# Optimization experiments

Measured on AMD Instinct MI355X. Metric: run time of the kernel, lower is better.

Reference implementation:

```python
import jax, jax.numpy as jnp
import numpy as np
from jax import lax

# NOTE: ResidualConvBlock and SS2DChanelFirst are reconstructed from the repo's
# conventions: ResidualConvBlock = act(conv3x3 -> act -> conv3x3 + 1x1 skip);
# SS2DChanelFirst = standard VMamba SS2D (in_proj -> dw-conv3x3 -> SiLU ->
# 4-direction cross-scan selective scan -> cross-merge -> LayerNorm -> *SiLU(z)
# gate -> out_proj) operating on NCHW tensors.

B, CIN, H, W = 4, 6, 64, 64
DM, DI, K, N, R, NL, GROUPS = 72, 144, 4, 8, 4, 2, 12


def conv2d(x, w, b=None, groups=1):
    out = lax.conv_general_dilated(x, w, (1, 1), 'SAME',
                                   dimension_numbers=('NCHW', 'OIHW', 'NCHW'),
                                   feature_group_count=groups)
    if b is not None:
        out = out + b[None, :, None, None]
    return out


def lrelu(x, s):
    return jnp.where(x >= 0, x, s * x)


def selective_scan(u, delta, A, Bs, Cs, D):
    # u, delta: (b,K,C,L); A: (K,C,N); Bs, Cs: (b,K,N,L); D: (K,C)
    b, k, c, l = u.shape
    n = A.shape[-1]
    ul = jnp.moveaxis(u, -1, 0)
    dl = jnp.moveaxis(delta, -1, 0)
    Bl = jnp.moveaxis(Bs, -1, 0)
    Cl = jnp.moveaxis(Cs, -1, 0)
    h0 = jnp.zeros((b, k, c, n), u.dtype)

    def step(h, xt):
        d_t, u_t, B_t, C_t = xt
        h = h * jnp.exp(d_t[..., None] * A) + (d_t * u_t)[..., None] * B_t[:, :, None, :]
        return h, jnp.einsum('bkcn,bkn->bkc', h, C_t)

    _, ys = lax.scan(step, h0, (dl, ul, Bl, Cl))
    return jnp.moveaxis(ys, 0, -1) + u * D[None, :, :, None]


def ss2d(x, in_w, dw_w, dw_b, xp_w, dtp_w, dtp_b, A_logs, Ds, ong, onb, op_w):
    b, dm, h_, w_ = x.shape
    l = h_ * w_
    xz = jnp.einsum('ec,bchw->behw', in_w, x)  # (b, 2*DI, h, w)
    xi, z = xz[:, :DI], xz[:, DI:]
    xi = jax.nn.silu(conv2d(xi, dw_w, dw_b, groups=DI))
    # cross-scan: row-major, col-major, and their reverses
    x0 = xi.reshape(b, DI, l)
    x1 = jnp.swapaxes(xi, 2, 3).reshape(b, DI, l)
    xs = jnp.stack([x0, x1, x0[..., ::-1], x1[..., ::-1]], axis=1)  # (b,4,DI,l)
    x_dbl = jnp.einsum('bkdl,kcd->bkcl', xs, xp_w)  # (b,4,R+2N,l)
    dts, Bs, Cs = x_dbl[:, :, :R], x_dbl[:, :, R:R + N], x_dbl[:, :, R + N:]
    dts = jnp.einsum('bkrl,kdr->bkdl', dts, dtp_w)
    delta = jax.nn.softplus(dts + dtp_b[None, :, :, None])
    A = -jnp.exp(A_logs).reshape(K, DI, N)
    ys = selective_scan(xs, delta, A, Bs, Cs, Ds.reshape(K, DI))  # (b,4,DI,l)
    # cross-merge
    y = ys[:, 0] + ys[:, 2, :, ::-1]
    yt = ys[:, 1] + ys[:, 3, :, ::-1]
    y = y + jnp.swapaxes(yt.reshape(b, DI, w_, h_), 2, 3).reshape(b, DI, l)
    y = jnp.swapaxes(y, 1, 2)  # (b,l,DI)
    mu = y.mean(-1, keepdims=True)
    var = ((y - mu) ** 2).mean(-1, keepdims=True)
    y = (y - mu) / jnp.sqrt(var + 1e-5) * ong + onb
    y = y * jax.nn.silu(jnp.swapaxes(z.reshape(b, DI, l), 1, 2))
    out = jnp.einsum('bld,ed->ble', y, op_w)  # (b,l,DM)
    return jnp.swapaxes(out, 1, 2).reshape(b, dm, h_, w_)


def groupnorm(x, g, bta, groups):
    b, c, h_, w_ = x.shape
    xg = x.reshape(b, groups, c // groups, h_ * w_)
    mu = xg.mean((2, 3), keepdims=True)
    var = ((xg - mu) ** 2).mean((2, 3), keepdims=True)
    xg = (xg - mu) / jnp.sqrt(var + 1e-5)
    return xg.reshape(b, c, h_, w_) * g[None, :, None, None] + bta[None, :, None, None]


def setup_inputs() -> dict:
    key = jax.random.key(0)
    ks = iter(jax.random.split(key, 32))
    nrm = lambda shp, s=0.05: jax.random.normal(next(ks), shp, jnp.float32) * s
    inp = {
        'image': jax.random.normal(next(ks), (B, CIN, H, W), jnp.float32),
        'cb_w1': nrm((DM, CIN, 3, 3), 0.1), 'cb_b1': nrm((DM,), 0.02),
        'cb_w2': nrm((DM, DM, 3, 3), 0.05), 'cb_b2': nrm((DM,), 0.02),
        'cb_ws': nrm((DM, CIN, 1, 1), 0.1), 'cb_bs': nrm((DM,), 0.02),
        'in_w': nrm((NL, 2 * DI, DM), 0.05),
        'dw_w': nrm((NL, DI, 1, 3, 3), 0.1), 'dw_b': nrm((NL, DI), 0.02),
        'xp_w': nrm((NL, K, R + 2 * N, DI), 0.05),
        'dtp_w': nrm((NL, K, DI, R), 0.1), 'dtp_b': nrm((NL, K, DI), 0.1),
        'A_logs': nrm((NL, K * DI, N), 0.5),
        'Ds': jnp.ones((NL, K * DI), jnp.float32) + nrm((NL, K * DI), 0.05),
        'ong': jnp.ones((NL, DI), jnp.float32), 'onb': jnp.zeros((NL, DI), jnp.float32),
        'op_w': nrm((NL, DM, DI), 0.05),
        'gn_g': jnp.ones((NL, DM), jnp.float32), 'gn_b': jnp.zeros((NL, DM), jnp.float32),
        'l1_w': nrm((NL, DM, DM), 0.1), 'l1_b': nrm((NL, DM), 0.02),
        'l2_w': nrm((NL, DM, DM), 0.1), 'l2_b': nrm((NL, DM), 0.02),
        'shrink_w': nrm((CIN, DM, 3, 3), 0.05), 'shrink_b': nrm((CIN,), 0.02),
    }
    return inp


def reference(image, cb_w1, cb_b1, cb_w2, cb_b2, cb_ws, cb_bs, in_w, dw_w, dw_b,
              xp_w, dtp_w, dtp_b, A_logs, Ds, ong, onb, op_w, gn_g, gn_b,
              l1_w, l1_b, l2_w, l2_b, shrink_w, shrink_b):
    # ResidualConvBlock (expand 6 -> 72), leaky_relu
    h = lrelu(conv2d(image, cb_w1, cb_b1), 0.01)
    h = conv2d(h, cb_w2, cb_b2) + conv2d(image, cb_ws, cb_bs)
    x = lrelu(h, 0.01)
    for i in range(NL):
        x = ss2d(x, in_w[i], dw_w[i], dw_b[i], xp_w[i], dtp_w[i], dtp_b[i],
                 A_logs[i], Ds[i], ong[i], onb[i], op_w[i])
        x = groupnorm(x, gn_g[i], gn_b[i], GROUPS)
        x = jnp.einsum('oc,bchw->bohw', l1_w[i], x) + l1_b[i][None, :, None, None]
        x = lrelu(x, 0.04)
        x = jnp.einsum('oc,bchw->bohw', l2_w[i], x) + l2_b[i][None, :, None, None]
    x = conv2d(x, shrink_w, shrink_b)
    return jax.nn.sigmoid(x)
```

## Files before the change

### kernel.cpp

```cpp
#include <hip/hip_runtime.h>
#include <math.h>

#define BB 4
#define CI 6
#define LL 4096
#define DMC 72
#define DIC 144
#define KD 4
#define NS 8
#define RD 4
#define NLAYER 2
#define GRP 12
#define NCH 256
#define TS 16
#define SP 72
#define PPN (66*SP)
#define L2E 1.4426950408889634f

__device__ __forceinline__ float sigmoidf_(float x){ return 1.f/(1.f+__expf(-x)); }
__device__ __forceinline__ float siluf_(float x){ return x*sigmoidf_(x); }
__device__ __forceinline__ float softplusf_(float x){
  return fmaxf(x,0.f) + __logf(1.f + __expf(-fabsf(x)));
}

__device__ __forceinline__ int padidx(int p){ return SP*(p>>6) + (p&63) + SP + 4; }

#define LOAD9(ip, a) do { \
  a[0]=(ip)[-SP-1]; a[1]=(ip)[-SP]; a[2]=(ip)[-SP+1]; \
  a[3]=(ip)[-1];    a[4]=(ip)[0];   a[5]=(ip)[1];     \
  a[6]=(ip)[SP-1];  a[7]=(ip)[SP];  a[8]=(ip)[SP+1];  } while(0)

__device__ __forceinline__ void load6(const float* __restrict__ base, float v[6]){
  v[0] = base[-1];
  float4 f = *(const float4*)base;
  v[1]=f.x; v[2]=f.y; v[3]=f.z; v[4]=f.w;
  v[5] = base[4];
}

__global__ void k_halo(float* __restrict__ pads, int nplanes){
  int plane = blockIdx.x;
  if (plane >= nplanes) return;
  int t = threadIdx.x;
  if (t >= 260) return;
  float* pl = pads + (size_t)plane*PPN;
  int row, col;
  if (t < 132){
    row = (t < 66) ? 0 : 65;
    col = 3 + (t % 66);
  } else {
    int j = t - 132;
    col = (j < 64) ? 3 : 68;
    row = 1 + (j & 63);
  }
  pl[row*SP + col] = 0.f;
}

__global__ void k_pad_img(const float* __restrict__ img, float* __restrict__ img_pad){
  int idx = blockIdx.x*256 + threadIdx.x;
  if (idx >= BB*CI*LL) return;
  int p = idx & 4095; int bc = idx >> 12;
  img_pad[(size_t)bc*PPN + padidx(p)] = img[idx];
}

__global__ void k_conv1(const float* __restrict__ img_pad, const float* __restrict__ w,
                        const float* __restrict__ bias, float* __restrict__ tmp_pad){
  int bid = blockIdx.x;
  int tile = bid & 3; int r = bid >> 2; int o = r % DMC; int b = r / DMC;
  int p0 = tile*1024 + threadIdx.x*4;
  int pb = padidx(p0);
  float bv = bias[o];
  float acc[4] = {bv,bv,bv,bv};
  #pragma unroll
  for (int ic=0; ic<CI; ++ic){
    const float* ip = img_pad + (size_t)(b*CI+ic)*PPN + pb;
    const float* wr = w + (o*CI+ic)*9;
    #pragma unroll
    for (int rr=0; rr<3; ++rr){
      float v[6]; load6(ip + (rr-1)*SP, v);
      float w0=wr[rr*3], w1=wr[rr*3+1], w2v=wr[rr*3+2];
      #pragma unroll
      for (int q=0;q<4;++q) acc[q] += v[q]*w0 + v[q+1]*w1 + v[q+2]*w2v;
    }
  }
  #pragma unroll
  for (int q=0;q<4;++q) acc[q] = acc[q] >= 0.f ? acc[q] : 0.01f*acc[q];
  *(float4*)(tmp_pad + (size_t)(b*DMC+o)*PPN + pb) = make_float4(acc[0],acc[1],acc[2],acc[3]);
}

__global__ void k_conv2init(const float* __restrict__ img, const float* __restrict__ b2,
                            const float* __restrict__ wsc, const float* __restrict__ bsc,
                            float* __restrict__ xout){
  int bid = blockIdx.x;
  int t = bid & 15; int r = bid >> 4; int og = r % 18; int b = r / 18;
  int p = t*256 + threadIdx.x;
  float acc[4];
  #pragma unroll
  for (int j=0;j<4;++j) acc[j] = b2[og*4+j] + bsc[og*4+j];
  #pragma unroll
  for (int ic=0; ic<CI; ++ic){
    float v = img[((b*CI+ic)<<12)+p];
    #pragma unroll
    for (int j=0;j<4;++j) acc[j] += v * wsc[(og*4+j)*CI+ic];
  }
  #pragma unroll
  for (int j=0;j<4;++j)
    xout[((b*DMC+og*4+j)<<12)+p] = acc[j];
}

__global__ void k_conv2(const float* __restrict__ tmp_pad,
                        const float* __restrict__ w2, float* __restrict__ xout){
  int bid = blockIdx.x;
  int t = bid & 15; int r = bid >> 4; int og = r % 18; r /= 18;
  int icg = r & 1; int b = r >> 1;
  int p = t*256 + threadIdx.x;
  int pb = padidx(p);
  float acc[4] = {0.f,0.f,0.f,0.f};
  const float* ipb = tmp_pad + (size_t)b*DMC*PPN + pb;
  const float* wb  = w2 + (size_t)(og*4)*DMC*9;
  #pragma unroll 2
  for (int ii=0; ii<36; ++ii){
    int ic = icg*36 + ii;
    const float* ip = ipb + (size_t)ic*PPN;
    float a[9]; LOAD9(ip, a);
    const float* wp = wb + ic*9;
    #pragma unroll
    for (int j=0;j<4;++j){
      float s = 0.f;
      #pragma unroll
      for (int q=0;q<9;++q) s += a[q]*wp[(size_t)j*DMC*9 + q];
      acc[j] += s;
    }
  }
  #pragma unroll
  for (int j=0;j<4;++j)
    atomicAdd(xout + ((b*DMC+og*4+j)<<12)+p, acc[j]);
}

__global__ void k_xz(const float* __restrict__ x, const float* __restrict__ inw,
                     float* __restrict__ xz_pad, float* __restrict__ z_t, int relu){
  int bid = blockIdx.x;
  int t = bid & 15; int r = bid >> 4; int eg = r % 36; int b = r / 36;
  int p = t*256 + threadIdx.x;
  float acc[8] = {0.f,0.f,0.f,0.f,0.f,0.f,0.f,0.f};
  for (int c0=0; c0<DMC; c0+=4){
    float a[4];
    #pragma unroll
    for (int q=0;q<4;++q) a[q] = x[((b*DMC+c0+q)<<12)+p];
    if (relu){
      #pragma unroll
      for (int q=0;q<4;++q) a[q] = a[q] >= 0.f ? a[q] : 0.01f*a[q];
    }
    #pragma unroll
    for (int j=0;j<8;++j){
      float4 w = *(const float4*)(inw + (eg*8+j)*DMC + c0);
      acc[j] += a[0]*w.x + a[1]*w.y + a[2]*w.z + a[3]*w.w;
    }
  }
  if (eg < 18){
    int pb = padidx(p);
    #pragma unroll
    for (int j=0;j<8;++j) xz_pad[(size_t)(b*DIC+eg*8+j)*PPN + pb] = acc[j];
  } else {
    float* zb = z_t + ((size_t)b*LL+p)*DIC + (eg*8-DIC);
    *(float4*)(zb)   = make_float4(acc[0],acc[1],acc[2],acc[3]);
    *(float4*)(zb+4) = make_float4(acc[4],acc[5],acc[6],acc[7]);
  }
}

__global__ void k_dw(const float* __restrict__ xz_pad, const float* __restrict__ dww,
                     const float* __restrict__ dwb, float* __restrict__ xi_t){
  int bid = blockIdx.x;
  int tile = bid & 3; int r = bid >> 2; int c = r % DIC; int b = r / DIC;
  int p0 = tile*1024 + threadIdx.x*4;
  int pb = padidx(p0);
  const float* ip = xz_pad + (size_t)(b*DIC+c)*PPN + pb;
  const float* wp = dww + c*9;
  float bv = dwb[c];
  float acc[4] = {bv,bv,bv,bv};
  #pragma unroll
  for (int rr=0; rr<3; ++rr){
    float v[6]; load6(ip + (rr-1)*SP, v);
    float w0=wp[rr*3], w1=wp[rr*3+1], w2v=wp[rr*3+2];
    #pragma unroll
    for (int q=0;q<4;++q) acc[q] += v[q]*w0 + v[q+1]*w1 + v[q+2]*w2v;
  }
  #pragma unroll
  for (int q=0;q<4;++q)
    xi_t[((size_t)b*LL+p0+q)*DIC + c] = siluf_(acc[q]);
}

__global__ void k_xdbl(const float* __restrict__ xi_t, const float* __restrict__ xpw,
                       float* __restrict__ xdbl){
  int bid = blockIdx.x;
  int t = bid & 15; int r = bid >> 4;
  int kk = r & 3; r >>= 2; int part = r & 3; int b = r >> 2;
  int p = t*256 + threadIdx.x;
  const float* xib = xi_t + ((size_t)b*LL + p)*DIC;
  const float* wk = xpw + (size_t)(kk*20 + part*5)*DIC;
  float acc[5] = {0.f,0.f,0.f,0.f,0.f};
  for (int d=0; d<DIC; d+=4){
    float4 v = *(const float4*)(xib + d);
    #pragma unroll
    for (int c=0;c<5;++c){
      float4 w = *(const float4*)(wk + (size_t)c*DIC + d);
      acc[c] += v.x*w.x + v.y*w.y + v.z*w.z + v.w*w.w;
    }
  }
  float* dst = xdbl + ((size_t)(b*KD+kk)*LL + p)*20 + part*5;
  #pragma unroll
  for (int c=0;c<5;++c) dst[c] = acc[c];
}

__device__ __forceinline__ void scan_decode(int idx, int& b, int& k, int& ch, int& c){
  c = idx % DIC;
  int r = idx / DIC;
  ch = r % NCH;
  r /= NCH;
  k = r & 3; b = r >> 2;
}

__device__ __forceinline__ void scan_affine(int k, int ch, int& ps0, int& sk){
  int l0 = ch*TS;
  if (k == 0){ ps0 = l0; sk = 1; }
  else if (k == 1){ ps0 = ((l0 & 63) << 6) | (l0 >> 6); sk = 64; }
  else if (k == 2){ ps0 = (LL-1) - l0; sk = -1; }
  else { int m0 = (LL-1) - l0; ps0 = ((m0 & 63) << 6) | (m0 >> 6); sk = -64; }
}

__global__ void k_p1(const float* __restrict__ xi_t, const float* __restrict__ xdbl,
                     const float* __restrict__ dtpw, const float* __restrict__ dtpb,
                     const float* __restrict__ alog,
                     float* __restrict__ cumA, float* __restrict__ hp){
  int idx = blockIdx.x*256 + threadIdx.x;
  if (idx >= BB*KD*NCH*DIC) return;
  int b,k,ch,c; scan_decode(idx,b,k,ch,c);
  float Arow[NS];
  #pragma unroll
  for (int n=0;n<NS;++n) Arow[n] = -__expf(alog[(k*DIC+c)*NS+n]) * L2E;
  float4 wdt = *(const float4*)(dtpw + (k*DIC+c)*RD);
  float bdt = dtpb[k*DIC+c];
  int ps0, sk; scan_affine(k, ch, ps0, sk);
  const float* row = xdbl + (size_t)(b*KD+k)*LL*20 + (size_t)ps0*20;
  const float* up  = xi_t + (size_t)b*LL*DIC + c + (size_t)ps0*DIC;
  long rstep = (long)sk*20;
  long ustep = (long)sk*DIC;
  float h[NS];
  #pragma unroll
  for (int n=0;n<NS;++n) h[n]=0.f;
  float sumd = 0.f;
  #pragma unroll 4
  for (int t=0; t<TS; ++t){
    float4 q0 = *(const float4*)(row);
    float4 q1 = *(const float4*)(row+4);
    float4 q2 = *(const float4*)(row+8);
    float u = *up;
    float dt = bdt + q0.x*wdt.x + q0.y*wdt.y + q0.z*wdt.z + q0.w*wdt.w;
    dt = softplusf_(dt);
    sumd += dt;
    float du = dt*u;
    float Bv[NS] = {q1.x,q1.y,q1.z,q1.w,q2.x,q2.y,q2.z,q2.w};
    #pragma unroll
    for (int n=0;n<NS;++n)
      h[n] = h[n]*exp2f(dt*Arow[n]) + du*Bv[n];
    row += rstep; up += ustep;
  }
  size_t base = ((size_t)((b*KD+k)*NCH + ch)*NS)*DIC + c;
  #pragma unroll
  for (int n=0;n<NS;++n) hp[base + n*DIC] = h[n];
  #pragma unroll
  for (int n=0;n<NS;++n) cumA[base + n*DIC] = exp2f(sumd*Arow[n]);
}

__global__ void k_p2(float* __restrict__ cumA, float* __restrict__ hp,
                     float* __restrict__ gnstats){
  if (blockIdx.x == 0 && threadIdx.x < 2*BB*GRP) gnstats[threadIdx.x] = 0.f;
  int idx = blockIdx.x*256 + threadIdx.x;
  if (idx >= BB*KD*NS*DIC) return;
  int c = idx % DIC; int n = (idx/DIC) % NS; int bk = idx/(DIC*NS);
  float h = 0.f;
  #pragma unroll 8
  for (int ch=0; ch<NCH; ++ch){
    size_t base = ((size_t)(bk*NCH+ch)*NS + n)*DIC + c;
    float a = cumA[base];
    float pp = hp[base];
    cumA[base] = 0.f;
    hp[base] = h;
    h = a*h + pp;
  }
}

__global__ void k_p3(const float* __restrict__ xi_t, const float* __restrict__ xdbl,
                     const float* __restrict__ dtpw, const float* __restrict__ dtpb,
                     const float* __restrict__ alog, const float* __restrict__ Dsv,
                     const float* __restrict__ hin, float* __restrict__ y_t){
  int idx = blockIdx.x*256 + threadIdx.x;
  if (idx >= BB*KD*NCH*DIC) return;
  int b,k,ch,c; scan_decode(idx,b,k,ch,c);
  float Arow[NS];
  #pragma unroll
  for (int n=0;n<NS;++n) Arow[n] = -__expf(alog[(k*DIC+c)*NS+n]) * L2E;
  float4 wdt = *(const float4*)(dtpw + (k*DIC+c)*RD);
  float bdt = dtpb[k*DIC+c];
  float Dv = Dsv[k*DIC+c];
  int ps0, sk; scan_affine(k, ch, ps0, sk);
  const float* row = xdbl + (size_t)(b*KD+k)*LL*20 + (size_t)ps0*20;
  const float* up  = xi_t + (size_t)b*LL*DIC + c + (size_t)ps0*DIC;
  float* yp        = y_t  + (size_t)b*LL*DIC + c + (size_t)ps0*DIC;
  long rstep = (long)sk*20;
  long ustep = (long)sk*DIC;
  float h[NS];
  size_t base = ((size_t)((b*KD+k)*NCH + ch)*NS)*DIC + c;
  #pragma unroll
  for (int n=0;n<NS;++n) h[n] = hin[base + n*DIC];
  #pragma unroll 4
  for (int t=0; t<TS; ++t){
    float4 q0 = *(const float4*)(row);
    float4 q1 = *(const float4*)(row+4);
    float4 q2 = *(const float4*)(row+8);
    float4 q3 = *(const float4*)(row+12);
    float4 q4 = *(const float4*)(row+16);
    float u = *up;
    float dt = bdt + q0.x*wdt.x + q0.y*wdt.y + q0.z*wdt.z + q0.w*wdt.w;
    dt = softplusf_(dt);
    float du = dt*u;
    float Bv[NS] = {q1.x,q1.y,q1.z,q1.w,q2.x,q2.y,q2.z,q2.w};
    float Cv[NS] = {q3.x,q3.y,q3.z,q3.w,q4.x,q4.y,q4.z,q4.w};
    float y = 0.f;
    #pragma unroll
    for (int n=0;n<NS;++n){
      h[n] = h[n]*exp2f(dt*Arow[n]) + du*Bv[n];
      y += h[n]*Cv[n];
    }
    y += u*Dv;
    atomicAdd(yp, y);
    row += rstep; up += ustep; yp += ustep;
  }
}

__global__ void k_lnz(float* __restrict__ y_t, const float* __restrict__ z_t,
                      const float* __restrict__ ong, const float* __restrict__ onb,
                      float* __restrict__ xzero){
  int gid = blockIdx.x*256 + threadIdx.x;
  xzero[gid] = 0.f;
  if (gid < (int)(BB*DMC*LL - BB*LL*64)) xzero[gid + BB*LL*64] = 0.f;
  int wid = gid >> 6;
  int lane = gid & 63;
  if (wid >= BB*LL) return;
  size_t rb = (size_t)wid * DIC;
  float v0 = y_t[rb + lane];
  float v1 = y_t[rb + 64 + lane];
  float v2 = (lane < 16) ? y_t[rb + 128 + lane] : 0.f;
  float s = v0 + v1 + v2;
  float q = v0*v0 + v1*v1 + v2*v2;
  #pragma unroll
  for (int o=32; o>0; o>>=1){ s += __shfl_xor(s,o,64); q += __shfl_xor(q,o,64); }
  float mu = s*(1.f/DIC);
  float var = q*(1.f/DIC) - mu*mu;
  float rs = rsqrtf(var + 1e-5f);
  float z0 = z_t[rb + lane];
  y_t[rb + lane] = ((v0-mu)*rs*ong[lane] + onb[lane]) * siluf_(z0);
  float z1 = z_t[rb + 64 + lane];
  y_t[rb + 64 + lane] = ((v1-mu)*rs*ong[64+lane] + onb[64+lane]) * siluf_(z1);
  if (lane < 16){
    float z2 = z_t[rb + 128 + lane];
    y_t[rb + 128 + lane] = ((v2-mu)*rs*ong[128+lane] + onb[128+lane]) * siluf_(z2);
  }
}

__global__ void k_oproj(const float* __restrict__ yn, const float* __restrict__ opw,
                        float* __restrict__ xout){
  __shared__ float ly[72*65];
  int bid = blockIdx.x;
  int dhalf = bid & 1; int r = bid >> 1;
  int tile = r & 63; int b = r >> 6;
  int pstart = tile*64;
  const float* src = yn + ((size_t)b*LL + pstart)*DIC + dhalf*72;
  for (int i = threadIdx.x; i < 64*72; i += 512){
    int px = i / 72; int d = i - px*72;
    ly[d*65 + px] = src[(size_t)px*DIC + d];
  }
  __syncthreads();
  int px = threadIdx.x & 63;
  int ocg = __builtin_amdgcn_readfirstlane(threadIdx.x >> 6);
  float acc[9];
  #pragma unroll
  for (int j=0;j<9;++j) acc[j]=0.f;
  const float* wb = opw + (size_t)ocg*9*DIC + dhalf*72;
  #pragma unroll 4
  for (int d=0; d<72; ++d){
    float a = ly[d*65 + px];
    #pragma unroll
    for (int j=0;j<9;++j) acc[j] += a * wb[(size_t)j*DIC + d];
  }
  #pragma unroll
  for (int j=0;j<9;++j)
    atomicAdd(xout + ((size_t)(b*DMC + ocg*9 + j)<<12) + pstart + px, acc[j]);
}

__global__ void k_gnA(const float* __restrict__ x, float* __restrict__ stats){
  __shared__ float s1[256], s2[256];
  int bid = blockIdx.x;
  int t = bid & 15; int r = bid >> 4; int gr = r % GRP; int b = r / GRP;
  float ls=0.f, lq=0.f;
  #pragma unroll
  for (int it=0; it<6; ++it){
    int i = t*1536 + it*256 + threadIdx.x;
    int c = gr*6 + (i>>12); int p = i & 4095;
    float v = x[((size_t)(b*DMC+c)<<12)+p];
    ls += v; lq += v*v;
  }
  s1[threadIdx.x]=ls; s2[threadIdx.x]=lq; __syncthreads();
  for (int s=128; s>0; s>>=1){
    if (threadIdx.x < s){ s1[threadIdx.x]+=s1[threadIdx.x+s]; s2[threadIdx.x]+=s2[threadIdx.x+s]; }
    __syncthreads();
  }
  if (threadIdx.x == 0){
    atomicAdd(stats + (b*GRP+gr)*2,     s1[0]);
    atomicAdd(stats + (b*GRP+gr)*2 + 1, s2[0]);
  }
}

__global__ void k_dense1(const float* __restrict__ xin, const float* __restrict__ gnstats,
                         const float* __restrict__ gng, const float* __restrict__ gnb,
                         const float* __restrict__ w, const float* __restrict__ bias,
                         float* __restrict__ xout){
  __shared__ float As[DMC], Bs[DMC];
  int bid = blockIdx.x;
  int t = bid & 15; int r = bid >> 4; int eg = r % 18; int b = r / 18;
  if (threadIdx.x < DMC){
    int c = threadIdx.x; int gr = c/6;
    float s = gnstats[(b*GRP+gr)*2];
    float q = gnstats[(b*GRP+gr)*2 + 1];
    const float inv = 1.f/(6.f*LL);
    float mu = s*inv;
    float var = q*inv - mu*mu;
    float rs = rsqrtf(var + 1e-5f);
    float A = rs*gng[c];
    As[c] = A;
    Bs[c] = gnb[c] - mu*A;
  }
  __syncthreads();
  int p = t*256 + threadIdx.x;
  float acc[4];
  #pragma unroll
  for (int j=0;j<4;++j) acc[j] = bias[eg*4+j];
  for (int c0=0; c0<DMC; c0+=4){
    float a[4];
    #pragma unroll
    for (int q=0;q<4;++q){
      float v = xin[((size_t)(b*DMC+c0+q)<<12)+p];
      a[q] = v*As[c0+q] + Bs[c0+q];
    }
    #pragma unroll
    for (int j=0;j<4;++j){
      float4 w0 = *(const float4*)(w + (eg*4+j)*DMC + c0);
      acc[j] += a[0]*w0.x + a[1]*w0.y + a[2]*w0.z + a[3]*w0.w;
    }
  }
  #pragma unroll
  for (int j=0;j<4;++j)
    xout[((size_t)(b*DMC+eg*4+j)<<12)+p] = acc[j];
}

__global__ void k_dense2(const float* __restrict__ xin, const float* __restrict__ w,
                         const float* __restrict__ bias, float* __restrict__ xout,
                         float* __restrict__ pad_out){
  int bid = blockIdx.x;
  int t = bid & 15; int r = bid >> 4; int eg = r % 18; int b = r / 18;
  int p = t*256 + threadIdx.x;
  float acc[4];
  #pragma unroll
  for (int j=0;j<4;++j) acc[j] = bias[eg*4+j];
  for (int c0=0; c0<DMC; c0+=4){
    float a[4];
    #pragma unroll
    for (int q=0;q<4;++q){
      float v = xin[((size_t)(b*DMC+c0+q)<<12)+p];
      a[q] = v >= 0.f ? v : 0.04f*v;
    }
    #pragma unroll
    for (int j=0;j<4;++j){
      float4 w0 = *(const float4*)(w + (eg*4+j)*DMC + c0);
      acc[j] += a[0]*w0.x + a[1]*w0.y + a[2]*w0.z + a[3]*w0.w;
    }
  }
  int pb = padidx(p);
  #pragma unroll
  for (int j=0;j<4;++j){
    xout[((size_t)(b*DMC+eg*4+j)<<12)+p] = acc[j];
    if (pad_out) pad_out[(size_t)(b*DMC+eg*4+j)*PPN + pb] = acc[j];
  }
}

__global__ void k_shrinkA(const float* __restrict__ x_pad, const float* __restrict__ w,
                          float* __restrict__ pacc){
  int bid = blockIdx.x;
  int t = bid & 15; int r = bid >> 4; int icg = r % 24; int b = r / 24;
  int p = t*256 + threadIdx.x;
  int pb = padidx(p);
  float acc[6] = {0.f,0.f,0.f,0.f,0.f,0.f};
  const float* ipb = x_pad + (size_t)b*DMC*PPN + pb;
  #pragma unroll
  for (int ii=0; ii<3; ++ii){
    int ic = icg*3 + ii;
    const float* ip = ipb + (size_t)ic*PPN;
    float a[9]; LOAD9(ip, a);
    #pragma unroll
    for (int o=0;o<6;++o){
      const float* wp = w + (o*DMC+ic)*9;
      float s = 0.f;
      #pragma unroll
      for (int q=0;q<9;++q) s += a[q]*wp[q];
      acc[o] += s;
    }
  }
  #pragma unroll
  for (int o=0;o<6;++o)
    atomicAdd(pacc + ((size_t)(b*CI+o)<<12)+p, acc[o]);
}

__global__ void k_sig(const float* __restrict__ pacc, const float* __restrict__ bias,
                      float* __restrict__ out){
  int idx = blockIdx.x*256 + threadIdx.x;
  if (idx >= BB*CI*LL) return;
  int o = (idx>>12) % CI;
  out[idx] = sigmoidf_(pacc[idx] + bias[o]);
}

extern "C" void kernel_launch(void* const* d_in, const int* in_sizes, int n_in,
                              void* d_out, int out_size, void* d_ws, size_t ws_size,
                              hipStream_t stream){
  const float* image = (const float*)d_in[0];
  const float* cb_w1 = (const float*)d_in[1];
  const float* cb_b1 = (const float*)d_in[2];
  const float* cb_w2 = (const float*)d_in[3];
  const float* cb_b2 = (const float*)d_in[4];
  const float* cb_ws = (const float*)d_in[5];
  const float* cb_bs = (const float*)d_in[6];
  const float* in_w  = (const float*)d_in[7];
  const float* dw_w  = (const float*)d_in[8];
  const float* dw_b  = (const float*)d_in[9];
  const float* xp_w  = (const float*)d_in[10];
  const float* dtp_w = (const float*)d_in[11];
  const float* dtp_b = (const float*)d_in[12];
  const float* A_logs= (const float*)d_in[13];
  const float* Ds    = (const float*)d_in[14];
  const float* ong   = (const float*)d_in[15];
  const float* onb   = (const float*)d_in[16];
  const float* op_w  = (const float*)d_in[17];
  const float* gn_g  = (const float*)d_in[18];
  const float* gn_b  = (const float*)d_in[19];
  const float* l1_w  = (const float*)d_in[20];
  const float* l1_b  = (const float*)d_in[21];
  const float* l2_w  = (const float*)d_in[22];
  const float* l2_b  = (const float*)d_in[23];
  const float* sh_w  = (const float*)d_in[24];
  const float* sh_b  = (const float*)d_in[25];

  const size_t SZ_X  = (size_t)BB*DMC*LL;
  const size_t SZ_C  = (size_t)BB*DIC*LL;
  const size_t SZ_XD = (size_t)BB*KD*20*LL;
  const size_t SZ_HP = (size_t)BB*KD*NCH*NS*DIC;
  const size_t SZ_IP = (size_t)BB*CI*PPN;
  const size_t SZ_TP = (size_t)BB*DMC*PPN;
  const size_t SZ_ZP = (size_t)BB*DIC*PPN;

  float* ws = (float*)d_ws;
  size_t off = 0;
  float* x     = ws + off; off += SZ_X;
  float* tmp   = ws + off; off += SZ_X;
  float* z_t   = ws + off; off += SZ_C;
  float* xi_t  = ws + off; off += SZ_C;
  float* xdbl  = ws + off; off += SZ_XD;
  float* cumA  = ws + off; off += SZ_HP;
  float* hp    = ws + off; off += SZ_HP;
  float* pads  = ws + off;
  float* img_pad = pads;
  float* tmp_pad = img_pad + SZ_IP;
  float* xz_pad  = tmp_pad + SZ_TP;
  off += SZ_IP + SZ_TP + SZ_ZP;
  float* gnstats = ws + off; off += 2*BB*GRP;
  if (ws_size < off*sizeof(float)) return;
  float* y_t = cumA;

  dim3 blk(256);
  const int NPLANES = BB*CI + BB*DMC + BB*DIC;

  k_halo<<<dim3(NPLANES), blk, 0, stream>>>(pads, NPLANES);
  k_pad_img<<<dim3(BB*CI*16), blk, 0, stream>>>(image, img_pad);
  k_conv1<<<dim3(BB*DMC*4), blk, 0, stream>>>(img_pad, cb_w1, cb_b1, tmp_pad);
  k_conv2init<<<dim3(BB*18*16), blk, 0, stream>>>(image, cb_b2, cb_ws, cb_bs, x);
  k_conv2<<<dim3(BB*2*18*16), blk, 0, stream>>>(tmp_pad, cb_w2, x);

  for (int i=0; i<NLAYER; ++i){
    const float* in_w_i  = in_w  + (size_t)i*2*DIC*DMC;
    const float* dw_w_i  = dw_w  + (size_t)i*DIC*9;
    const float* dw_b_i  = dw_b  + (size_t)i*DIC;
    const float* xp_w_i  = xp_w  + (size_t)i*KD*20*DIC;
    const float* dtp_w_i = dtp_w + (size_t)i*KD*DIC*RD;
    const float* dtp_b_i = dtp_b + (size_t)i*KD*DIC;
    const float* alog_i  = A_logs+ (size_t)i*KD*DIC*NS;
    const float* Ds_i    = Ds    + (size_t)i*KD*DIC;
    const float* ong_i   = ong   + (size_t)i*DIC;
    const float* onb_i   = onb   + (size_t)i*DIC;
    const float* op_w_i  = op_w  + (size_t)i*DMC*DIC;
    const float* gn_g_i  = gn_g  + (size_t)i*DMC;
    const float* gn_b_i  = gn_b  + (size_t)i*DMC;
    const float* l1_w_i  = l1_w  + (size_t)i*DMC*DMC;
    const float* l1_b_i  = l1_b  + (size_t)i*DMC;
    const float* l2_w_i  = l2_w  + (size_t)i*DMC*DMC;
    const float* l2_b_i  = l2_b  + (size_t)i*DMC;

    k_xz  <<<dim3(BB*36*16), blk, 0, stream>>>(x, in_w_i, xz_pad, z_t, (i==0)?1:0);
    k_dw  <<<dim3(BB*DIC*4), blk, 0, stream>>>(xz_pad, dw_w_i, dw_b_i, xi_t);
    k_xdbl<<<dim3(BB*4*KD*16), blk, 0, stream>>>(xi_t, xp_w_i, xdbl);
    k_p1  <<<dim3(BB*KD*NCH*DIC/256), blk, 0, stream>>>(xi_t, xdbl, dtp_w_i, dtp_b_i, alog_i, cumA, hp);
    k_p2  <<<dim3(BB*KD*NS*DIC/256), blk, 0, stream>>>(cumA, hp, gnstats);
    k_p3  <<<dim3(BB*KD*NCH*DIC/256), blk, 0, stream>>>(xi_t, xdbl, dtp_w_i, dtp_b_i, alog_i, Ds_i, hp, y_t);
    k_lnz <<<dim3(BB*LL/4), blk, 0, stream>>>(y_t, z_t, ong_i, onb_i, x);
    k_oproj<<<dim3(BB*64*2), dim3(512), 0, stream>>>(y_t, op_w_i, x);
    k_gnA <<<dim3(BB*GRP*16), blk, 0, stream>>>(x, gnstats);
    k_dense1<<<dim3(BB*18*16), blk, 0, stream>>>(x, gnstats, gn_g_i, gn_b_i, l1_w_i, l1_b_i, tmp);
    k_dense2<<<dim3(BB*18*16), blk, 0, stream>>>(tmp, l2_w_i, l2_b_i, x,
                                                 (i==NLAYER-1) ? tmp_pad : (float*)nullptr);
  }

  hipMemsetAsync(tmp, 0, (size_t)BB*CI*LL*sizeof(float), stream);
  k_shrinkA<<<dim3(BB*24*16), blk, 0, stream>>>(tmp_pad, sh_w, tmp);
  k_sig<<<dim3((BB*CI*LL+255)/256), blk, 0, stream>>>(tmp, sh_b, (float*)d_out);
}
```

Baseline: 498.1 us.

## Pair forward/reverse scan directions in phase 3 and store chunk dt sums

Phase 3 now handles a direction and its reversed twin in one thread, since both cover the same positions. Their outputs are summed in registers and each position gets one atomic add instead of two. Phase 1 stores only the per-chunk sum of dt instead of eight cumulative-decay values, and phase 2 recomputes the exp2 itself. This cuts global writes and the zeroing of the cumA buffer. y_t moves to its own buffer, zeroed in phase 1, and phase 3 uses more registers (two state sets plus a 16-entry accumulator), which may lower occupancy.

```diff
diff --git a/kernel.cpp b/kernel.cpp
--- a/kernel.cpp
+++ b/kernel.cpp
@@ -230,9 +230,13 @@
 __global__ void k_p1(const float* __restrict__ xi_t, const float* __restrict__ xdbl,
                      const float* __restrict__ dtpw, const float* __restrict__ dtpb,
                      const float* __restrict__ alog,
-                     float* __restrict__ cumA, float* __restrict__ hp){
+                     float* __restrict__ cumdt, float* __restrict__ hp,
+                     float* __restrict__ y_t){
   int idx = blockIdx.x*256 + threadIdx.x;
   if (idx >= BB*KD*NCH*DIC) return;
+  const int NQ = BB*KD*NCH*DIC;
+  #pragma unroll
+  for (int j=0;j<4;++j) y_t[idx + (size_t)j*NQ] = 0.f;
   int b,k,ch,c; scan_decode(idx,b,k,ch,c);
   float Arow[NS];
   #pragma unroll
@@ -267,23 +271,24 @@
   size_t base = ((size_t)((b*KD+k)*NCH + ch)*NS)*DIC + c;
   #pragma unroll
   for (int n=0;n<NS;++n) hp[base + n*DIC] = h[n];
-  #pragma unroll
-  for (int n=0;n<NS;++n) cumA[base + n*DIC] = exp2f(sumd*Arow[n]);
-}
-
-__global__ void k_p2(float* __restrict__ cumA, float* __restrict__ hp,
-                     float* __restrict__ gnstats){
+  cumdt[((size_t)((b*KD+k)*NCH + ch))*DIC + c] = sumd;
+}
+
+__global__ void k_p2(const float* __restrict__ cumdt, float* __restrict__ hp,
+                     const float* __restrict__ alog, float* __restrict__ gnstats){
   if (blockIdx.x == 0 && threadIdx.x < 2*BB*GRP) gnstats[threadIdx.x] = 0.f;
   int idx = blockIdx.x*256 + threadIdx.x;
   if (idx >= BB*KD*NS*DIC) return;
   int c = idx % DIC; int n = (idx/DIC) % NS; int bk = idx/(DIC*NS);
+  int k = bk & 3;
+  float Arow = -__expf(alog[(k*DIC+c)*NS+n]) * L2E;
   float h = 0.f;
-  #pragma unroll 8
+  #pragma unroll 4
   for (int ch=0; ch<NCH; ++ch){
+    float sd = cumdt[((size_t)(bk*NCH+ch))*DIC + c];
+    float a = exp2f(sd*Arow);
     size_t base = ((size_t)(bk*NCH+ch)*NS + n)*DIC + c;
-    float a = cumA[base];
     float pp = hp[base];
-    cumA[base] = 0.f;
     hp[base] = h;
     h = a*h + pp;
   }
@@ -294,47 +299,91 @@
                      const float* __restrict__ alog, const float* __restrict__ Dsv,
                      const float* __restrict__ hin, float* __restrict__ y_t){
   int idx = blockIdx.x*256 + threadIdx.x;
-  if (idx >= BB*KD*NCH*DIC) return;
-  int b,k,ch,c; scan_decode(idx,b,k,ch,c);
-  float Arow[NS];
-  #pragma unroll
-  for (int n=0;n<NS;++n) Arow[n] = -__expf(alog[(k*DIC+c)*NS+n]) * L2E;
-  float4 wdt = *(const float4*)(dtpw + (k*DIC+c)*RD);
-  float bdt = dtpb[k*DIC+c];
-  float Dv = Dsv[k*DIC+c];
-  int ps0, sk; scan_affine(k, ch, ps0, sk);
-  const float* row = xdbl + (size_t)(b*KD+k)*LL*20 + (size_t)ps0*20;
-  const float* up  = xi_t + (size_t)b*LL*DIC + c + (size_t)ps0*DIC;
-  float* yp        = y_t  + (size_t)b*LL*DIC + c + (size_t)ps0*DIC;
-  long rstep = (long)sk*20;
-  long ustep = (long)sk*DIC;
-  float h[NS];
-  size_t base = ((size_t)((b*KD+k)*NCH + ch)*NS)*DIC + c;
-  #pragma unroll
-  for (int n=0;n<NS;++n) h[n] = hin[base + n*DIC];
-  #pragma unroll 4
+  if (idx >= BB*2*NCH*DIC) return;
+  int c = idx % DIC;
+  int r = idx / DIC;
+  int ch = r % NCH; r /= NCH;
+  int pr = r & 1; int b = r >> 1;
+  int kA = pr, kB = pr | 2;
+  int chB = NCH-1-ch;
+  int st = pr ? 64 : 1;
+  int l0 = ch*TS;
+  int p0 = pr ? (((l0 & 63) << 6) | (l0 >> 6)) : l0;
+
+  float ArowA[NS], ArowB[NS];
+  #pragma unroll
+  for (int n=0;n<NS;++n){
+    ArowA[n] = -__expf(alog[(kA*DIC+c)*NS+n]) * L2E;
+    ArowB[n] = -__expf(alog[(kB*DIC+c)*NS+n]) * L2E;
+  }
+  float4 wdtA = *(const float4*)(dtpw + (kA*DIC+c)*RD);
+  float4 wdtB = *(const float4*)(dtpw + (kB*DIC+c)*RD);
+  float bdtA = dtpb[kA*DIC+c];
+  float bdtB = dtpb[kB*DIC+c];
+  float Dsum = Dsv[kA*DIC+c] + Dsv[kB*DIC+c];
+  const float* xdA = xdbl + (size_t)(b*KD+kA)*LL*20;
+  const float* xdB = xdbl + (size_t)(b*KD+kB)*LL*20;
+  const float* up = xi_t + (size_t)b*LL*DIC + c;
+  float* yb = y_t + (size_t)b*LL*DIC + c;
+  float hA[NS], hB[NS];
+  size_t baseA = ((size_t)((b*KD+kA)*NCH + ch)*NS)*DIC + c;
+  size_t baseB = ((size_t)((b*KD+kB)*NCH + chB)*NS)*DIC + c;
+  #pragma unroll
+  for (int n=0;n<NS;++n){ hA[n] = hin[baseA + n*DIC]; hB[n] = hin[baseB + n*DIC]; }
+  float yacc[TS];
+  #pragma unroll
+  for (int j=0;j<TS;++j) yacc[j] = 0.f;
+
+  #pragma unroll
   for (int t=0; t<TS; ++t){
-    float4 q0 = *(const float4*)(row);
-    float4 q1 = *(const float4*)(row+4);
-    float4 q2 = *(const float4*)(row+8);
-    float4 q3 = *(const float4*)(row+12);
-    float4 q4 = *(const float4*)(row+16);
-    float u = *up;
-    float dt = bdt + q0.x*wdt.x + q0.y*wdt.y + q0.z*wdt.z + q0.w*wdt.w;
-    dt = softplusf_(dt);
-    float du = dt*u;
-    float Bv[NS] = {q1.x,q1.y,q1.z,q1.w,q2.x,q2.y,q2.z,q2.w};
-    float Cv[NS] = {q3.x,q3.y,q3.z,q3.w,q4.x,q4.y,q4.z,q4.w};
-    float y = 0.f;
-    #pragma unroll
-    for (int n=0;n<NS;++n){
-      h[n] = h[n]*exp2f(dt*Arow[n]) + du*Bv[n];
-      y += h[n]*Cv[n];
-    }
-    y += u*Dv;
-    atomicAdd(yp, y);
-    row += rstep; up += ustep; yp += ustep;
-  }
+    int pA = p0 + t*st;
+    int pB = p0 + (TS-1-t)*st;
+    {
+      const float* row = xdA + (size_t)pA*20;
+      float4 q0 = *(const float4*)(row);
+      float4 q1 = *(const float4*)(row+4);
+      float4 q2 = *(const float4*)(row+8);
+      float4 q3 = *(const float4*)(row+12);
+      float4 q4 = *(const float4*)(row+16);
+      float u = up[(size_t)pA*DIC];
+      float dt = bdtA + q0.x*wdtA.x + q0.y*wdtA.y + q0.z*wdtA.z + q0.w*wdtA.w;
+      dt = softplusf_(dt);
+      float du = dt*u;
+      float Bv[NS] = {q1.x,q1.y,q1.z,q1.w,q2.x,q2.y,q2.z,q2.w};
+      float Cv[NS] = {q3.x,q3.y,q3.z,q3.w,q4.x,q4.y,q4.z,q4.w};
+      float y = 0.f;
+      #pragma unroll
+      for (int n=0;n<NS;++n){
+        hA[n] = hA[n]*exp2f(dt*ArowA[n]) + du*Bv[n];
+        y += hA[n]*Cv[n];
+      }
+      yacc[t] += y + u*Dsum;
+    }
+    {
+      const float* row = xdB + (size_t)pB*20;
+      float4 q0 = *(const float4*)(row);
+      float4 q1 = *(const float4*)(row+4);
+      float4 q2 = *(const float4*)(row+8);
+      float4 q3 = *(const float4*)(row+12);
+      float4 q4 = *(const float4*)(row+16);
+      float u = up[(size_t)pB*DIC];
+      float dt = bdtB + q0.x*wdtB.x + q0.y*wdtB.y + q0.z*wdtB.z + q0.w*wdtB.w;
+      dt = softplusf_(dt);
+      float du = dt*u;
+      float Bv[NS] = {q1.x,q1.y,q1.z,q1.w,q2.x,q2.y,q2.z,q2.w};
+      float Cv[NS] = {q3.x,q3.y,q3.z,q3.w,q4.x,q4.y,q4.z,q4.w};
+      float y = 0.f;
+      #pragma unroll
+      for (int n=0;n<NS;++n){
+        hB[n] = hB[n]*exp2f(dt*ArowB[n]) + du*Bv[n];
+        y += hB[n]*Cv[n];
+      }
+      yacc[TS-1-t] += y;
+    }
+  }
+  #pragma unroll
+  for (int j=0;j<TS;++j)
+    atomicAdd(yb + (size_t)(p0 + j*st)*DIC, yacc[j]);
 }
 
 __global__ void k_lnz(float* __restrict__ y_t, const float* __restrict__ z_t,
@@ -560,6 +609,7 @@
   const size_t SZ_X  = (size_t)BB*DMC*LL;
   const size_t SZ_C  = (size_t)BB*DIC*LL;
   const size_t SZ_XD = (size_t)BB*KD*20*LL;
+  const size_t SZ_CD = (size_t)BB*KD*NCH*DIC;
   const size_t SZ_HP = (size_t)BB*KD*NCH*NS*DIC;
   const size_t SZ_IP = (size_t)BB*CI*PPN;
   const size_t SZ_TP = (size_t)BB*DMC*PPN;
@@ -572,7 +622,8 @@
   float* z_t   = ws + off; off += SZ_C;
   float* xi_t  = ws + off; off += SZ_C;
   float* xdbl  = ws + off; off += SZ_XD;
-  float* cumA  = ws + off; off += SZ_HP;
+  float* y_t   = ws + off; off += SZ_C;
+  float* cumdt = ws + off; off += SZ_CD;
   float* hp    = ws + off; off += SZ_HP;
   float* pads  = ws + off;
   float* img_pad = pads;
@@ -581,7 +632,6 @@
   off += SZ_IP + SZ_TP + SZ_ZP;
   float* gnstats = ws + off; off += 2*BB*GRP;
   if (ws_size < off*sizeof(float)) return;
-  float* y_t = cumA;
 
   dim3 blk(256);
   const int NPLANES = BB*CI + BB*DMC + BB*DIC;
@@ -614,9 +664,9 @@
     k_xz  <<<dim3(BB*36*16), blk, 0, stream>>>(x, in_w_i, xz_pad, z_t, (i==0)?1:0);
     k_dw  <<<dim3(BB*DIC*4), blk, 0, stream>>>(xz_pad, dw_w_i, dw_b_i, xi_t);
     k_xdbl<<<dim3(BB*4*KD*16), blk, 0, stream>>>(xi_t, xp_w_i, xdbl);
-    k_p1  <<<dim3(BB*KD*NCH*DIC/256), blk, 0, stream>>>(xi_t, xdbl, dtp_w_i, dtp_b_i, alog_i, cumA, hp);
-    k_p2  <<<dim3(BB*KD*NS*DIC/256), blk, 0, stream>>>(cumA, hp, gnstats);
-    k_p3  <<<dim3(BB*KD*NCH*DIC/256), blk, 0, stream>>>(xi_t, xdbl, dtp_w_i, dtp_b_i, alog_i, Ds_i, hp, y_t);
+    k_p1  <<<dim3(BB*KD*NCH*DIC/256), blk, 0, stream>>>(xi_t, xdbl, dtp_w_i, dtp_b_i, alog_i, cumdt, hp, y_t);
+    k_p2  <<<dim3(BB*KD*NS*DIC/256), blk, 0, stream>>>(cumdt, hp, alog_i, gnstats);
+    k_p3  <<<dim3(BB*2*NCH*DIC/256), blk, 0, stream>>>(xi_t, xdbl, dtp_w_i, dtp_b_i, alog_i, Ds_i, hp, y_t);
     k_lnz <<<dim3(BB*LL/4), blk, 0, stream>>>(y_t, z_t, ong_i, onb_i, x);
     k_oproj<<<dim3(BB*64*2), dim3(512), 0, stream>>>(y_t, op_w_i, x);
     k_gnA <<<dim3(BB*GRP*16), blk, 0, stream>>>(x, gnstats);
```

New measurement: 598.9 us. 20.2% more time.
